# Performance work log

Hardware: AMD Instinct MI355X
Metric: run time of the kernel (lower is better)

## Reference

```python
import jax, jax.numpy as jnp
import numpy as np

N_NODES = 100000
N_EDGES = 1600000
IN_CH = 128
HID_CH = 128
OUT_CH = 128
EDGE_DIM = 16
EPS = 1e-12


def _xavier(key, shape):
    fan_in, fan_out = shape[1], shape[0]
    a = jnp.sqrt(6.0 / (fan_in + fan_out))
    # torch Linear weight is [out, in]; we store transposed [in, out] for x @ W
    return jax.random.uniform(key, (shape[1], shape[0]), minval=-a, maxval=a, dtype=jnp.float32)


def setup_inputs() -> dict:
    key = jax.random.key(0)
    ks = jax.random.split(key, 8)
    x = jax.random.normal(ks[0], (N_NODES, IN_CH), dtype=jnp.float32)
    edge_index = jax.random.randint(ks[1], (2, N_EDGES), 0, N_NODES, dtype=jnp.int64)
    edge_attr = jax.random.normal(ks[2], (N_EDGES, EDGE_DIM), dtype=jnp.float32)
    # layer 1: message Linear(in+edge_dim -> hid), update Linear(in+hid -> hid)
    w_msg1 = _xavier(ks[3], (HID_CH, IN_CH + EDGE_DIM))
    b_msg1 = jnp.zeros((HID_CH,), jnp.float32)
    w_upd1 = _xavier(ks[4], (HID_CH, IN_CH + HID_CH))
    b_upd1 = jnp.zeros((HID_CH,), jnp.float32)
    bias1 = jnp.zeros((HID_CH,), jnp.float32)
    # layer 2: message Linear(hid+edge_dim -> out), update Linear(hid+out -> out)
    w_msg2 = _xavier(ks[5], (OUT_CH, HID_CH + EDGE_DIM))
    b_msg2 = jnp.zeros((OUT_CH,), jnp.float32)
    w_upd2 = _xavier(ks[6], (OUT_CH, HID_CH + OUT_CH))
    b_upd2 = jnp.zeros((OUT_CH,), jnp.float32)
    bias2 = jnp.zeros((OUT_CH,), jnp.float32)
    return {
        "x": x, "edge_index": edge_index, "edge_attr": edge_attr,
        "w_msg1": w_msg1, "b_msg1": b_msg1, "w_upd1": w_upd1, "b_upd1": b_upd1, "bias1": bias1,
        "w_msg2": w_msg2, "b_msg2": b_msg2, "w_upd2": w_upd2, "b_upd2": b_upd2, "bias2": bias2,
    }


def _layer(x, src, dst, edge_attr, w_msg, b_msg, w_upd, b_upd, bias):
    n = x.shape[0]
    # message: gather source node feats, concat edge feats, Linear + ReLU
    msg_in = jnp.concatenate([x[src], edge_attr], axis=1)        # [E, in+edge_dim]
    msg = jax.nn.relu(msg_in @ w_msg + b_msg)                     # [E, out]
    # scatter-mean aggregate at destination nodes
    summed = jax.ops.segment_sum(msg, dst, num_segments=n)        # [N, out]
    cnt = jax.ops.segment_sum(jnp.ones((msg.shape[0], 1), msg.dtype), dst, num_segments=n)
    agg = summed / jnp.maximum(cnt, 1.0)
    # update: concat self feats + aggregated, Linear
    out = jnp.concatenate([x, agg], axis=1) @ w_upd + b_upd       # [N, out]
    # F.normalize(p=2, dim=-1)
    norm = jnp.linalg.norm(out, axis=-1, keepdims=True)
    out = out / jnp.maximum(norm, EPS)
    return out + bias


def reference(x, edge_index, edge_attr,
              w_msg1, b_msg1, w_upd1, b_upd1, bias1,
              w_msg2, b_msg2, w_upd2, b_upd2, bias2):
    src, dst = edge_index[0], edge_index[1]
    h = _layer(x, src, dst, edge_attr, w_msg1, b_msg1, w_upd1, b_upd1, bias1)
    h = jax.nn.relu(h)  # inter-layer ReLU (dropout p=0.0 is identity)
    h = _layer(h, src, dst, edge_attr, w_msg2, b_msg2, w_upd2, b_upd2, bias2)
    return h
```

## Files before the change

kernel.cpp:

```cpp
#include <hip/hip_runtime.h>
#include <stdint.h>

#define N_NODES 100000
#define N_EDGES 1600000
#define CH 128
#define EDGE_DIM 16
#define KUPD 256
#define NPW 8

typedef __attribute__((ext_vector_type(8))) short short8v;
typedef __attribute__((ext_vector_type(4))) float f32x4;

__device__ __forceinline__ float bf2f(ushort u) {
  union { uint i; float f; } c; c.i = ((uint)u) << 16; return c.f;
}
__device__ __forceinline__ ushort f2bf(float f) {
  union { float f; uint i; } c; c.f = f;
  return (ushort)((c.i + 0x7FFFu + ((c.i >> 16) & 1u)) >> 16);
}
__device__ __forceinline__ float ldf(const void* p, int f32, size_t i) {
  return f32 ? ((const float*)p)[i] : bf2f(((const ushort*)p)[i]);
}
__device__ __forceinline__ float2 ld2(const void* p, int f32, size_t pi) {
  if (f32) return ((const float2*)p)[pi];
  uint u = ((const uint*)p)[pi];
  return make_float2(bf2f((ushort)(u & 0xFFFF)), bf2f((ushort)(u >> 16)));
}
__device__ __forceinline__ float4 ld4(const void* p, int f32, size_t qi) {
  if (f32) return ((const float4*)p)[qi];
  uint2 u = ((const uint2*)p)[qi];
  float4 r;
  r.x = bf2f((ushort)(u.x & 0xFFFF)); r.y = bf2f((ushort)(u.x >> 16));
  r.z = bf2f((ushort)(u.y & 0xFFFF)); r.w = bf2f((ushort)(u.y >> 16));
  return r;
}
__device__ __forceinline__ int resolve_f32(int x_sel, const int* flags) {
  return (x_sel == 2) ? 1 : (x_sel == 1 ? flags[1] : 0);
}
__device__ __forceinline__ int kmap(int MAP, int g, int j, int step) {
  return MAP ? (step * 32 + 8 * g + j)
             : (step * 32 + 16 * (j >> 2) + 4 * g + (j & 3));
}

__global__ __launch_bounds__(256) void detect_kernel(const int* __restrict__ ei,
                                                     const ushort* __restrict__ xu,
                                                     const ushort* __restrict__ eau,
                                                     const ushort* __restrict__ wu,
                                                     int* __restrict__ flags) {
  int any = 0, fx = 0, fe = 0, fw = 0;
  for (int i = threadIdx.x; i < 4096; i += 256) any |= ei[2 * i + 1];
  for (int i = threadIdx.x; i < 16384; i += 256) {
    fx |= (((xu[2 * i] >> 7) & 0xFF) == 0xFF);
    fe |= (((eau[2 * i] >> 7) & 0xFF) == 0xFF);
  }
  for (int i = threadIdx.x; i < 8192; i += 256) {
    fw |= (((wu[2 * i] >> 7) & 0xFF) == 0xFF);
  }
  if (any) atomicOr(flags + 0, 1);
  if (fx)  atomicOr(flags + 1, 1);
  if (fe)  atomicOr(flags + 2, 1);
  if (fw)  atomicOr(flags + 3, 1);
}

__global__ __launch_bounds__(64) void mfma_probe(int* __restrict__ flags) {
  __shared__ ushort A[16 * 32];
  __shared__ ushort B[32 * 16];
  const int lane = threadIdx.x;
  for (int idx = lane; idx < 512; idx += 64) {
    int i = idx >> 5, k = idx & 31;
    A[idx] = f2bf((float)((i * 5 + k * 3) % 13 - 6));
    int k2 = idx >> 4, c = idx & 15;
    B[idx] = f2bf((float)((k2 * 7 + c * 11) % 15 - 7));
  }
  __syncthreads();
  const int col = lane & 15, g = lane >> 4;
  float cr[4];
#pragma unroll
  for (int r = 0; r < 4; ++r) {
    int row = g * 4 + r;
    float s = 0.f;
    for (int k = 0; k < 32; ++k) s += bf2f(A[row * 32 + k]) * bf2f(B[k * 16 + col]);
    cr[r] = s;
  }
  int win = 2;
  for (int MAP = 0; MAP < 2; ++MAP) {
    if (win != 2) break;
    short8v a, b;
#pragma unroll
    for (int j = 0; j < 8; ++j) {
      int k = kmap(MAP, g, j, 0);
      a[j] = (short)A[(lane & 15) * 32 + k];
      b[j] = (short)B[k * 16 + col];
    }
    f32x4 z = {0.f, 0.f, 0.f, 0.f};
    f32x4 d = __builtin_amdgcn_mfma_f32_16x16x32_bf16(a, b, z, 0, 0, 0);
    int good = 1;
#pragma unroll
    for (int r = 0; r < 4; ++r) good &= (d[r] == cr[r]);
    if (__all(good)) win = MAP;
  }
  if (lane == 0) flags[4] = win;
}

__device__ __forceinline__ void load_edge(const int* __restrict__ ei, int i32, int e,
                                          int& s, int& d) {
  if (i32) { s = ei[e]; d = ei[N_EDGES + e]; }
  else     { s = ei[2 * e]; d = ei[2 * N_EDGES + 2 * e]; }
  s = min(max(s, 0), N_NODES - 1);
  d = min(max(d, 0), N_NODES - 1);
}

__global__ __launch_bounds__(256) void count_kernel(const int* __restrict__ ei,
                                                    const int* __restrict__ flags,
                                                    int* __restrict__ cnt) {
  int e = blockIdx.x * 256 + threadIdx.x;
  if (e >= N_EDGES) return;
  int d = flags[0] ? ei[N_EDGES + e] : ei[2 * N_EDGES + 2 * e];
  d = min(max(d, 0), N_NODES - 1);
  atomicAdd(&cnt[d], 1);
}

__global__ __launch_bounds__(1024) void scan_kernel(const int* __restrict__ cnt,
                                                    int* __restrict__ rowptr) {
  __shared__ int part[1024];
  const int t = threadIdx.x;
  const int CHUNK = (N_NODES + 1023) / 1024;
  int base = t * CHUNK;
  int lim = min(base + CHUNK, N_NODES);
  int s = 0;
  for (int i = base; i < lim; ++i) s += cnt[i];
  part[t] = s;
  __syncthreads();
  for (int off = 1; off < 1024; off <<= 1) {
    int v = (t >= off) ? part[t - off] : 0;
    __syncthreads();
    part[t] += v;
    __syncthreads();
  }
  int excl = (t == 0) ? 0 : part[t - 1];
  for (int i = base; i < lim; ++i) { rowptr[i] = excl; excl += cnt[i]; }
  if (t == 1023) rowptr[N_NODES] = part[1023];
}

__global__ __launch_bounds__(256) void scatter_kernel(const int* __restrict__ ei,
                                                      const int* __restrict__ flags,
                                                      const int* __restrict__ rowptr,
                                                      int* __restrict__ fill,
                                                      int2* __restrict__ sev) {
  int e = blockIdx.x * 256 + threadIdx.x;
  if (e >= N_EDGES) return;
  int s, d;
  load_edge(ei, flags[0], e, s, d);
  int pos = atomicAdd(&fill[d], 1);
  sev[rowptr[d] + pos] = make_int2(s, e);
}

__global__ __launch_bounds__(256) void wshuf_all(const void* __restrict__ wu1,
                                                 const void* __restrict__ wu2,
                                                 const void* __restrict__ wm1,
                                                 const void* __restrict__ wm2,
                                                 const int* __restrict__ flags,
                                                 ushort* __restrict__ ou1,
                                                 ushort* __restrict__ ou2,
                                                 ushort* __restrict__ om1,
                                                 ushort* __restrict__ om2,
                                                 ushort* __restrict__ oz1,
                                                 ushort* __restrict__ oz2) {
  const int MAP = flags[4], wf = flags[3];
  if (MAP == 2) return;
  int tid = blockIdx.x * 256 + threadIdx.x;
  if (tid >= 13312) return;
  int gg = tid >> 6, lane = tid & 63;
  int col16 = lane & 15, g = lane >> 4;
  if (gg >= 192) {
    int l = gg - 192;
    const void* W = (l < 8) ? wm1 : wm2;
    ushort* dst = (l < 8) ? oz1 : oz2;
    int t = l & 7;
#pragma unroll
    for (int j = 0; j < 8; ++j) {
      int k = kmap(MAP, g, j, 0);
      ushort v = (k < 16) ? f2bf(ldf(W, wf, (size_t)(CH + k) * CH + t * 16 + col16)) : (ushort)0;
      dst[(size_t)t * 512 + lane * 8 + j] = v;
    }
    return;
  }
  const void* W; ushort* dst; int t, step, ts;
  if (gg < 64)       { W = wu1; dst = ou1; int l = gg;       t = l >> 3; step = l & 7; ts = t * 8 + step; }
  else if (gg < 128) { W = wu2; dst = ou2; int l = gg - 64;  t = l >> 3; step = l & 7; ts = t * 8 + step; }
  else if (gg < 160) { W = wm1; dst = om1; int l = gg - 128; t = l >> 2; step = l & 3; ts = t * 4 + step; }
  else               { W = wm2; dst = om2; int l = gg - 160; t = l >> 2; step = l & 3; ts = t * 4 + step; }
  int col = t * 16 + col16;
#pragma unroll
  for (int j = 0; j < 8; ++j) {
    int k = kmap(MAP, g, j, step);
    dst[(size_t)ts * 512 + lane * 8 + j] = f2bf(ldf(W, wf, (size_t)k * CH + col));
  }
}

template <int MAP>
__device__ __forceinline__ void gemm_mfma_body(const void* __restrict__ x, int xf,
                                               const ushort* __restrict__ wshm,
                                               const void* __restrict__ bmsg, int wf,
                                               uint* __restrict__ ybf,
                                               int n0, int lane, char* lds) {
  const int srow = lane >> 2;
  const int q = lane & 3;
  {
    uint sw = (uint)((srow & 7) << 4);
#pragma unroll
    for (int i = 0; i < 8; ++i) {
      int qi = q + 4 * i;
      float4 v = ld4(x, xf, (size_t)(n0 + srow) * 32 + qi);
      uint2 pk;
      pk.x = (uint)f2bf(v.x) | ((uint)f2bf(v.y) << 16);
      pk.y = (uint)f2bf(v.z) | ((uint)f2bf(v.w) << 16);
      *(uint2*)(lds + (((uint)srow * 256u + (uint)qi * 8u) ^ sw)) = pk;
    }
  }
  asm volatile("s_waitcnt lgkmcnt(0)" ::: "memory");
  __builtin_amdgcn_sched_barrier(0);

  const int col = lane & 15, g = lane >> 4;
  const int ra = lane & 15;
  const uint asw = (uint)((ra & 7) << 4);
  f32x4 acc[8];
#pragma unroll
  for (int t = 0; t < 8; ++t) acc[t] = (f32x4){0.f, 0.f, 0.f, 0.f};

#pragma unroll
  for (int step = 0; step < 4; ++step) {
    short8v a;
    if (MAP) {
      uint byte = (uint)ra * 256u + (uint)(step * 32 + 8 * g) * 2u;
      *(uint4*)&a = *(const uint4*)(lds + (byte ^ asw));
    } else {
      uint b0 = (uint)ra * 256u + (uint)(step * 32 + 4 * g) * 2u;
      uint b1 = b0 + 32u;
      uint2 lo = *(const uint2*)(lds + (b0 ^ asw));
      uint2 hi = *(const uint2*)(lds + (b1 ^ asw));
      uint4 pk = make_uint4(lo.x, lo.y, hi.x, hi.y);
      *(uint4*)&a = pk;
    }
#pragma unroll
    for (int t = 0; t < 8; ++t) {
      short8v b = *(const short8v*)(wshm + ((size_t)(t * 4 + step) * 512 + lane * 8));
      acc[t] = __builtin_amdgcn_mfma_f32_16x16x32_bf16(a, b, acc[t], 0, 0, 0);
    }
  }

#pragma unroll
  for (int u = 0; u < 4; ++u) {
    float b0v = ldf(bmsg, wf, u * 32 + col);
    float b1v = ldf(bmsg, wf, u * 32 + 16 + col);
#pragma unroll
    for (int r = 0; r < 4; ++r) {
      uint pk = (uint)f2bf(acc[2 * u][r] + b0v) | ((uint)f2bf(acc[2 * u + 1][r] + b1v) << 16);
      ybf[(uint)(n0 + g * 4 + r) * 64u + (uint)(u * 16 + col)] = pk;
    }
  }
}

__device__ __forceinline__ void gemm_f32_body(const void* __restrict__ x, int xf,
                                              const void* __restrict__ W, int wf,
                                              const void* __restrict__ b,
                                              uint* __restrict__ ybf,
                                              int wave_n0, int lane, char* ldsc) {
  float* xs = (float*)ldsc;
  for (int c = 0; c < 2; ++c) {
    int n0 = wave_n0 + c * 8;
#pragma unroll
    for (int r = 0; r < NPW; ++r) {
      float2 a = ld2(x, xf, (size_t)(n0 + r) * 64 + lane);
      xs[r * 128 + 2 * lane]     = a.x;
      xs[r * 128 + 2 * lane + 1] = a.y;
    }
    asm volatile("s_waitcnt lgkmcnt(0)" ::: "memory");
    __builtin_amdgcn_sched_barrier(0);
    float acc0[NPW], acc1[NPW];
#pragma unroll
    for (int r = 0; r < NPW; ++r) { acc0[r] = 0.f; acc1[r] = 0.f; }
#pragma unroll 4
    for (int k = 0; k < CH; k += 2) {
      float2 w0 = ld2(W, wf, (size_t)k * 64 + lane);
      float2 w1 = ld2(W, wf, (size_t)(k + 1) * 64 + lane);
#pragma unroll
      for (int r = 0; r < NPW; ++r) {
        float2 a = *(const float2*)&xs[r * 128 + k];
        acc0[r] += a.x * w0.x;
        acc1[r] += a.x * w0.y;
        acc0[r] += a.y * w1.x;
        acc1[r] += a.y * w1.y;
      }
    }
    float2 bb = ld2(b, wf, lane);
#pragma unroll
    for (int r = 0; r < NPW; ++r) {
      uint pk = (uint)f2bf(acc0[r] + bb.x) | ((uint)f2bf(acc1[r] + bb.y) << 16);
      ybf[(uint)(n0 + r) * 64u + (uint)lane] = pk;
    }
  }
}

__global__ __launch_bounds__(256) void gemm_node(const void* __restrict__ x, int x_sel,
                                                 const ushort* __restrict__ wshm,
                                                 const void* __restrict__ W,
                                                 const void* __restrict__ b,
                                                 const int* __restrict__ flags,
                                                 uint* __restrict__ ybf) {
  __shared__ char lds[16384];
  const int wave = threadIdx.x >> 6;
  const int lane = threadIdx.x & 63;
  const int wid = blockIdx.x * 4 + wave;
  if (wid >= N_NODES / 16) return;
  const int n0 = wid * 16;
  const int xf = resolve_f32(x_sel, flags), wf = flags[3];
  const int MAP = flags[4];
  char* myl = lds + wave * 4096;
  if (MAP == 0)      gemm_mfma_body<0>(x, xf, wshm, b, wf, ybf, n0, lane, myl);
  else if (MAP == 1) gemm_mfma_body<1>(x, xf, wshm, b, wf, ybf, n0, lane, myl);
  else               gemm_f32_body(x, xf, W, wf, b, ybf, n0, lane, myl);
}

template <int MAP>
__device__ __forceinline__ void agg_mfma_body(const uint* __restrict__ ybf,
                                              const void* __restrict__ ea, int ef,
                                              const ushort* __restrict__ wze,
                                              const int* __restrict__ rowptr,
                                              const int2* __restrict__ sev,
                                              float* __restrict__ agg,
                                              int n, int lane) {
  const int col = lane & 15, g = lane >> 4;
  const int beg = rowptr[n], end = rowptr[n + 1];
  if (beg == end) {
    agg[(size_t)n * CH + (size_t)(2 * g) * 16 + col]     = 0.f;
    agg[(size_t)n * CH + (size_t)(2 * g + 1) * 16 + col] = 0.f;
    return;
  }
  short8v bfr[8];
#pragma unroll
  for (int t = 0; t < 8; ++t)
    bfr[t] = *(const short8v*)(wze + ((size_t)t * 512 + lane * 8));

  f32x4 acc[8];
#pragma unroll
  for (int t = 0; t < 8; ++t) acc[t] = (f32x4){0.f, 0.f, 0.f, 0.f};

  for (int j0 = beg; j0 < end; j0 += 16) {
    int jr = j0 + col;
    if (jr > end - 1) jr = end - 1;
    int2 p = sev[jr];
    int e = p.y;
    short8v a;
    if (MAP == 1) {
      if (g < 2) {
        float4 qa = ld4(ea, ef, (size_t)e * 4 + 2 * g);
        float4 qb = ld4(ea, ef, (size_t)e * 4 + 2 * g + 1);
        uint4 pk;
        pk.x = (uint)f2bf(qa.x) | ((uint)f2bf(qa.y) << 16);
        pk.y = (uint)f2bf(qa.z) | ((uint)f2bf(qa.w) << 16);
        pk.z = (uint)f2bf(qb.x) | ((uint)f2bf(qb.y) << 16);
        pk.w = (uint)f2bf(qb.z) | ((uint)f2bf(qb.w) << 16);
        *(uint4*)&a = pk;
      } else {
        *(uint4*)&a = make_uint4(0, 0, 0, 0);
      }
    } else {
      float4 q = ld4(ea, ef, (size_t)e * 4 + g);
      uint4 pk;
      pk.x = (uint)f2bf(q.x) | ((uint)f2bf(q.y) << 16);
      pk.y = (uint)f2bf(q.z) | ((uint)f2bf(q.w) << 16);
      pk.z = 0; pk.w = 0;
      *(uint4*)&a = pk;
    }
    f32x4 zz = {0.f, 0.f, 0.f, 0.f};
    f32x4 zf[8];
#pragma unroll
    for (int t = 0; t < 8; ++t)
      zf[t] = __builtin_amdgcn_mfma_f32_16x16x32_bf16(a, bfr[t], zz, 0, 0, 0);

    int myS = p.x;
#pragma unroll
    for (int r = 0; r < 4; ++r) {
      int slot = g * 4 + r;
      int s = __shfl(myS, slot);
      float valid = (j0 + slot < end) ? 1.f : 0.f;
#pragma unroll
      for (int u = 0; u < 4; ++u) {
        uint yu = ybf[(size_t)s * 64 + (size_t)u * 16 + col];
        float lo = bf2f((ushort)(yu & 0xFFFF));
        float hi = bf2f((ushort)(yu >> 16));
        acc[2 * u][r]     += valid * fmaxf(lo + zf[2 * u][r], 0.f);
        acc[2 * u + 1][r] += valid * fmaxf(hi + zf[2 * u + 1][r], 0.f);
      }
    }
  }
  float part[8];
#pragma unroll
  for (int t = 0; t < 8; ++t) {
    part[t] = (acc[t][0] + acc[t][1]) + (acc[t][2] + acc[t][3]);
    part[t] += __shfl_xor(part[t], 16);
    part[t] += __shfl_xor(part[t], 32);
  }
  agg[(size_t)n * CH + (size_t)(2 * g) * 16 + col]     = part[2 * g];
  agg[(size_t)n * CH + (size_t)(2 * g + 1) * 16 + col] = part[2 * g + 1];
}

__device__ __forceinline__ void agg_f32_body(const uint* __restrict__ ybf,
                                             const void* __restrict__ ea, int ef,
                                             const void* __restrict__ W, int wf,
                                             const int* __restrict__ rowptr,
                                             const int2* __restrict__ sev,
                                             float* __restrict__ agg,
                                             int n, int lane) {
  const int c0 = 2 * lane, c1 = c0 + 1;
  float wex[EDGE_DIM], wey[EDGE_DIM];
#pragma unroll
  for (int k = 0; k < EDGE_DIM; ++k) {
    wex[k] = ldf(W, wf, (size_t)(CH + k) * CH + c0);
    wey[k] = ldf(W, wf, (size_t)(CH + k) * CH + c1);
  }
  const int beg = rowptr[n], end = rowptr[n + 1];
  float acc0 = 0.f, acc1 = 0.f;
  for (int j = beg; j < end; ++j) {
    int2 p = sev[j];
    int s = __builtin_amdgcn_readfirstlane(p.x), e = __builtin_amdgcn_readfirstlane(p.y);
    uint yu = ybf[(size_t)s * 64 + lane];
    float4 q0 = ld4(ea, ef, (size_t)e * 4 + 0);
    float4 q1 = ld4(ea, ef, (size_t)e * 4 + 1);
    float4 q2 = ld4(ea, ef, (size_t)e * 4 + 2);
    float4 q3 = ld4(ea, ef, (size_t)e * 4 + 3);
    float av[16] = {q0.x, q0.y, q0.z, q0.w, q1.x, q1.y, q1.z, q1.w,
                    q2.x, q2.y, q2.z, q2.w, q3.x, q3.y, q3.z, q3.w};
    float z0 = 0.f, z1 = 0.f;
#pragma unroll
    for (int k = 0; k < EDGE_DIM; ++k) {
      z0 += av[k] * wex[k];
      z1 += av[k] * wey[k];
    }
    acc0 += fmaxf(bf2f((ushort)(yu & 0xFFFF)) + z0, 0.f);
    acc1 += fmaxf(bf2f((ushort)(yu >> 16)) + z1, 0.f);
  }
  agg[(size_t)n * CH + c0] = acc0;
  agg[(size_t)n * CH + c1] = acc1;
}

__global__ __launch_bounds__(256) void agg_csr(const uint* __restrict__ ybf,
                                               const void* __restrict__ ea,
                                               const ushort* __restrict__ wze,
                                               const void* __restrict__ W,
                                               const int* __restrict__ rowptr,
                                               const int2* __restrict__ sev,
                                               const int* __restrict__ flags,
                                               float* __restrict__ agg) {
  const int wave = threadIdx.x >> 6;
  const int lane = threadIdx.x & 63;
  const int n = blockIdx.x * 4 + wave;
  const int ef = flags[2], wf = flags[3], MAP = flags[4];
  if (MAP == 0)      agg_mfma_body<0>(ybf, ea, ef, wze, rowptr, sev, agg, n, lane);
  else if (MAP == 1) agg_mfma_body<1>(ybf, ea, ef, wze, rowptr, sev, agg, n, lane);
  else               agg_f32_body(ybf, ea, ef, W, wf, rowptr, sev, agg, n, lane);
}

template <int MAP>
__device__ __forceinline__ void upd_mfma_body(const void* __restrict__ x, int xf,
                                              const float* __restrict__ agg,
                                              const int* __restrict__ rowptr,
                                              const ushort* __restrict__ wsh,
                                              const void* __restrict__ bupd, int wf,
                                              const void* __restrict__ bias,
                                              float* __restrict__ out, int relu,
                                              int n0, int lane, char* lds) {
  const int srow = lane >> 2;
  const int q = lane & 3;
  {
    int c = rowptr[n0 + srow + 1] - rowptr[n0 + srow];
    float inv = 1.f / (float)(c > 1 ? c : 1);
    uint sw = (uint)((srow & 7) << 4);
#pragma unroll
    for (int i = 0; i < 8; ++i) {
      int qi = q + 4 * i;
      float4 v = ld4(x, xf, (size_t)(n0 + srow) * 32 + qi);
      uint2 pk;
      pk.x = (uint)f2bf(v.x) | ((uint)f2bf(v.y) << 16);
      pk.y = (uint)f2bf(v.z) | ((uint)f2bf(v.w) << 16);
      *(uint2*)(lds + (((uint)srow * 512u + (uint)qi * 8u) ^ sw)) = pk;
      float4 w = ((const float4*)agg)[(size_t)(n0 + srow) * 32 + qi];
      uint2 pk2;
      pk2.x = (uint)f2bf(w.x * inv) | ((uint)f2bf(w.y * inv) << 16);
      pk2.y = (uint)f2bf(w.z * inv) | ((uint)f2bf(w.w * inv) << 16);
      *(uint2*)(lds + (((uint)srow * 512u + 256u + (uint)qi * 8u) ^ sw)) = pk2;
    }
  }
  asm volatile("s_waitcnt lgkmcnt(0)" ::: "memory");
  __builtin_amdgcn_sched_barrier(0);

  const int col = lane & 15, g = lane >> 4;
  const int ra = lane & 15;
  const uint asw = (uint)((ra & 7) << 4);
  f32x4 acc[8];
#pragma unroll
  for (int t = 0; t < 8; ++t) acc[t] = (f32x4){0.f, 0.f, 0.f, 0.f};

#pragma unroll
  for (int step = 0; step < 8; ++step) {
    short8v a;
    if (MAP) {
      uint byte = (uint)ra * 512u + (uint)(step * 32 + 8 * g) * 2u;
      *(uint4*)&a = *(const uint4*)(lds + (byte ^ asw));
    } else {
      uint b0 = (uint)ra * 512u + (uint)(step * 32 + 4 * g) * 2u;
      uint b1 = b0 + 32u;
      uint2 lo = *(const uint2*)(lds + (b0 ^ asw));
      uint2 hi = *(const uint2*)(lds + (b1 ^ asw));
      uint4 pk = make_uint4(lo.x, lo.y, hi.x, hi.y);
      *(uint4*)&a = pk;
    }
#pragma unroll
    for (int t = 0; t < 8; ++t) {
      short8v b = *(const short8v*)(wsh + ((size_t)(t * 8 + step) * 512 + lane * 8));
      acc[t] = __builtin_amdgcn_mfma_f32_16x16x32_bf16(a, b, acc[t], 0, 0, 0);
    }
  }

  float bu[8], bi[8];
#pragma unroll
  for (int t = 0; t < 8; ++t) {
    bu[t] = ldf(bupd, wf, t * 16 + col);
    bi[t] = ldf(bias, wf, t * 16 + col);
  }
  float raw[8][4];
  float ss[4] = {0.f, 0.f, 0.f, 0.f};
#pragma unroll
  for (int t = 0; t < 8; ++t)
#pragma unroll
    for (int r = 0; r < 4; ++r) {
      float v = acc[t][r] + bu[t];
      raw[t][r] = v;
      ss[r] += v * v;
    }
#pragma unroll
  for (int r = 0; r < 4; ++r)
#pragma unroll
    for (int o = 1; o < 16; o <<= 1) ss[r] += __shfl_xor(ss[r], o);
#pragma unroll
  for (int r = 0; r < 4; ++r) {
    float inv = 1.0f / fmaxf(sqrtf(ss[r]), 1e-12f);
    int row = g * 4 + r;
#pragma unroll
    for (int t = 0; t < 8; ++t) {
      float o = raw[t][r] * inv + bi[t];
      if (relu) o = fmaxf(o, 0.f);
      out[(size_t)(n0 + row) * CH + t * 16 + col] = o;
    }
  }
}

__device__ __forceinline__ void upd_f32_body(const void* __restrict__ x, int xf,
                                             const float* __restrict__ agg,
                                             const int* __restrict__ rowptr,
                                             const void* __restrict__ W, int wf,
                                             const void* __restrict__ bupd,
                                             const void* __restrict__ bias,
                                             float* __restrict__ out, int relu,
                                             int wave_n0, int lane, char* ldsc) {
  float* xs = (float*)ldsc;
  for (int c = 0; c < 2; ++c) {
    int n0 = wave_n0 + c * 8;
#pragma unroll
    for (int r = 0; r < NPW; ++r) {
      int n = n0 + r;
      float2 a = ld2(x, xf, (size_t)n * 64 + lane);
      xs[r * 256 + 2 * lane]     = a.x;
      xs[r * 256 + 2 * lane + 1] = a.y;
      int cd = rowptr[n + 1] - rowptr[n];
      float inv = 1.f / (float)(cd > 1 ? cd : 1);
      xs[r * 256 + CH + 2 * lane]     = agg[(size_t)n * CH + 2 * lane] * inv;
      xs[r * 256 + CH + 2 * lane + 1] = agg[(size_t)n * CH + 2 * lane + 1] * inv;
    }
    asm volatile("s_waitcnt lgkmcnt(0)" ::: "memory");
    __builtin_amdgcn_sched_barrier(0);

    float acc0[NPW], acc1[NPW];
#pragma unroll
    for (int r = 0; r < NPW; ++r) { acc0[r] = 0.f; acc1[r] = 0.f; }
#pragma unroll 4
    for (int k = 0; k < KUPD; k += 2) {
      float2 w0 = ld2(W, wf, (size_t)k * 64 + lane);
      float2 w1 = ld2(W, wf, (size_t)(k + 1) * 64 + lane);
#pragma unroll
      for (int r = 0; r < NPW; ++r) {
        float2 a = *(const float2*)&xs[r * 256 + k];
        acc0[r] += a.x * w0.x;
        acc1[r] += a.x * w0.y;
        acc0[r] += a.y * w1.x;
        acc1[r] += a.y * w1.y;
      }
    }
    float2 b  = ld2(bupd, wf, lane);
    float2 bi = ld2(bias, wf, lane);
#pragma unroll
    for (int r = 0; r < NPW; ++r) {
      float r0 = acc0[r] + b.x;
      float r1 = acc1[r] + b.y;
      float sq = r0 * r0 + r1 * r1;
#pragma unroll
      for (int o = 32; o; o >>= 1) sq += __shfl_xor(sq, o);
      float innv = 1.0f / fmaxf(sqrtf(sq), 1e-12f);
      float o0 = r0 * innv + bi.x;
      float o1 = r1 * innv + bi.y;
      if (relu) { o0 = fmaxf(o0, 0.f); o1 = fmaxf(o1, 0.f); }
      size_t n = (size_t)(n0 + r);
      out[n * CH + 2 * lane]     = o0;
      out[n * CH + 2 * lane + 1] = o1;
    }
  }
}

__global__ __launch_bounds__(256) void upd_fused(const void* __restrict__ x, int x_sel,
                                                 const float* __restrict__ agg,
                                                 const int* __restrict__ rowptr,
                                                 const ushort* __restrict__ wsh,
                                                 const void* __restrict__ W,
                                                 const void* __restrict__ bupd,
                                                 const void* __restrict__ bias,
                                                 const int* __restrict__ flags,
                                                 float* __restrict__ out,
                                                 int relu) {
  __shared__ char lds[32768];
  const int wave = threadIdx.x >> 6;
  const int lane = threadIdx.x & 63;
  const int wid = blockIdx.x * 4 + wave;
  if (wid >= N_NODES / 16) return;
  const int n0 = wid * 16;
  const int xf = resolve_f32(x_sel, flags), wf = flags[3];
  const int MAP = flags[4];
  char* myl = lds + wave * 8192;
  if (MAP == 0)
    upd_mfma_body<0>(x, xf, agg, rowptr, wsh, bupd, wf, bias, out, relu, n0, lane, myl);
  else if (MAP == 1)
    upd_mfma_body<1>(x, xf, agg, rowptr, wsh, bupd, wf, bias, out, relu, n0, lane, myl);
  else
    upd_f32_body(x, xf, agg, rowptr, W, wf, bupd, bias, out, relu, n0, lane, myl);
}

extern "C" void kernel_launch(void* const* d_in, const int* in_sizes, int n_in,
                              void* d_out, int out_size, void* d_ws, size_t ws_size,
                              hipStream_t stream) {
  const void* x   = d_in[0];
  const int*  ei  = (const int*)d_in[1];
  const void* ea  = d_in[2];
  const void* wm1 = d_in[3];
  const void* bm1 = d_in[4];
  const void* wu1 = d_in[5];
  const void* bu1 = d_in[6];
  const void* bi1 = d_in[7];
  const void* wm2 = d_in[8];
  const void* bm2 = d_in[9];
  const void* wu2 = d_in[10];
  const void* bu2 = d_in[11];
  const void* bi2 = d_in[12];
  float* out = (float*)d_out;

  char* base = (char*)d_ws;
  size_t off = 0;
  auto alloc = [&](size_t b) { size_t o = off; off += (b + 255) & ~(size_t)255; return o; };
  size_t flags_o = alloc(32);
  size_t cnt_o   = alloc((size_t)N_NODES * 4);
  size_t fill_o  = alloc((size_t)N_NODES * 4);
  size_t zero_end = off;
  size_t rowp_o  = alloc((size_t)(N_NODES + 1) * 4);
  size_t sev_o   = alloc((size_t)N_EDGES * 8);
  size_t agg_o   = alloc((size_t)N_NODES * CH * 4);
  size_t y_o     = alloc((size_t)N_NODES * CH * 2);
  size_t wsh1_o  = alloc((size_t)4096 * 8 * 2);
  size_t wsh2_o  = alloc((size_t)4096 * 8 * 2);
  size_t wshm1_o = alloc((size_t)2048 * 8 * 2);
  size_t wshm2_o = alloc((size_t)2048 * 8 * 2);
  size_t wze1_o  = alloc((size_t)512 * 8 * 2);
  size_t wze2_o  = alloc((size_t)512 * 8 * 2);
  (void)ws_size; (void)n_in; (void)in_sizes; (void)out_size;

  int*    flags = (int*)(base + flags_o);
  int*    cntp  = (int*)(base + cnt_o);
  int*    fillp = (int*)(base + fill_o);
  int*    rowp  = (int*)(base + rowp_o);
  int2*   sevp  = (int2*)(base + sev_o);
  float*  aggp  = (float*)(base + agg_o);
  uint*   ybfp  = (uint*)(base + y_o);
  ushort* wsh1  = (ushort*)(base + wsh1_o);
  ushort* wsh2  = (ushort*)(base + wsh2_o);
  ushort* wshm1 = (ushort*)(base + wshm1_o);
  ushort* wshm2 = (ushort*)(base + wshm2_o);
  ushort* wze1  = (ushort*)(base + wze1_o);
  ushort* wze2  = (ushort*)(base + wze2_o);
  float*  hp    = out;

  hipMemsetAsync(base, 0, zero_end, stream);
  detect_kernel<<<1, 256, 0, stream>>>(ei, (const ushort*)x, (const ushort*)ea,
                                       (const ushort*)wm1, flags);
  mfma_probe<<<1, 64, 0, stream>>>(flags);
  count_kernel<<<(N_EDGES + 255) / 256, 256, 0, stream>>>(ei, flags, cntp);
  scan_kernel<<<1, 1024, 0, stream>>>(cntp, rowp);
  scatter_kernel<<<(N_EDGES + 255) / 256, 256, 0, stream>>>(ei, flags, rowp, fillp, sevp);
  wshuf_all<<<52, 256, 0, stream>>>(wu1, wu2, wm1, wm2, flags,
                                    wsh1, wsh2, wshm1, wshm2, wze1, wze2);

  const int agrid = N_NODES / 4;
  const int wgrid = (N_NODES / 16 + 3) / 4;

  gemm_node<<<wgrid, 256, 0, stream>>>(x, 1, wshm1, wm1, bm1, flags, ybfp);
  agg_csr<<<agrid, 256, 0, stream>>>(ybfp, ea, wze1, wm1, rowp, sevp, flags, aggp);
  upd_fused<<<wgrid, 256, 0, stream>>>(x, 1, aggp, rowp, wsh1, wu1, bu1, bi1, flags, hp, 1);

  gemm_node<<<wgrid, 256, 0, stream>>>(hp, 2, wshm2, wm2, bm2, flags, ybfp);
  agg_csr<<<agrid, 256, 0, stream>>>(ybfp, ea, wze2, wm2, rowp, sevp, flags, aggp);
  upd_fused<<<wgrid, 256, 0, stream>>>(hp, 2, aggp, rowp, wsh2, wu2, bu2, bi2, flags, out, 0);
}
```

Baseline: 1.007 ms.

## Process eight nodes per wave in aggregation and merge probe kernels

The CSR aggregation kernel now has each wave loop over eight consecutive destination nodes instead of one. The per-wave edge-weight fragments are loaded once and reused across those nodes, and the grid shrinks accordingly. Invalid padded edge slots are redirected to an extra zeroed sentinel row of the message buffer, and their edge-attribute operands are masked, so the per-element validity multiply goes away. The detect and MFMA-probe kernels are fused into one launch to save a kernel launch. The trade-off is fewer waves in flight, with per-wave load imbalance across nodes of different degree and serialised node latency.

```diff
diff --git a/kernel.cpp b/kernel.cpp
--- a/kernel.cpp
+++ b/kernel.cpp
@@ -42,11 +42,13 @@
              : (step * 32 + 16 * (j >> 2) + 4 * g + (j & 3));
 }
 
-__global__ __launch_bounds__(256) void detect_kernel(const int* __restrict__ ei,
-                                                     const ushort* __restrict__ xu,
-                                                     const ushort* __restrict__ eau,
-                                                     const ushort* __restrict__ wu,
-                                                     int* __restrict__ flags) {
+__global__ __launch_bounds__(256) void detect_probe(const int* __restrict__ ei,
+                                                    const ushort* __restrict__ xu,
+                                                    const ushort* __restrict__ eau,
+                                                    const ushort* __restrict__ wu,
+                                                    int* __restrict__ flags) {
+  __shared__ ushort A[16 * 32];
+  __shared__ ushort B[32 * 16];
   int any = 0, fx = 0, fe = 0, fw = 0;
   for (int i = threadIdx.x; i < 4096; i += 256) any |= ei[2 * i + 1];
   for (int i = threadIdx.x; i < 16384; i += 256) {
@@ -60,46 +62,43 @@
   if (fx)  atomicOr(flags + 1, 1);
   if (fe)  atomicOr(flags + 2, 1);
   if (fw)  atomicOr(flags + 3, 1);
-}
-
-__global__ __launch_bounds__(64) void mfma_probe(int* __restrict__ flags) {
-  __shared__ ushort A[16 * 32];
-  __shared__ ushort B[32 * 16];
-  const int lane = threadIdx.x;
-  for (int idx = lane; idx < 512; idx += 64) {
+  for (int idx = threadIdx.x; idx < 512; idx += 256) {
     int i = idx >> 5, k = idx & 31;
     A[idx] = f2bf((float)((i * 5 + k * 3) % 13 - 6));
     int k2 = idx >> 4, c = idx & 15;
     B[idx] = f2bf((float)((k2 * 7 + c * 11) % 15 - 7));
   }
   __syncthreads();
-  const int col = lane & 15, g = lane >> 4;
-  float cr[4];
-#pragma unroll
-  for (int r = 0; r < 4; ++r) {
-    int row = g * 4 + r;
-    float s = 0.f;
-    for (int k = 0; k < 32; ++k) s += bf2f(A[row * 32 + k]) * bf2f(B[k * 16 + col]);
-    cr[r] = s;
-  }
-  int win = 2;
-  for (int MAP = 0; MAP < 2; ++MAP) {
-    if (win != 2) break;
-    short8v a, b;
-#pragma unroll
-    for (int j = 0; j < 8; ++j) {
-      int k = kmap(MAP, g, j, 0);
-      a[j] = (short)A[(lane & 15) * 32 + k];
-      b[j] = (short)B[k * 16 + col];
-    }
-    f32x4 z = {0.f, 0.f, 0.f, 0.f};
-    f32x4 d = __builtin_amdgcn_mfma_f32_16x16x32_bf16(a, b, z, 0, 0, 0);
-    int good = 1;
-#pragma unroll
-    for (int r = 0; r < 4; ++r) good &= (d[r] == cr[r]);
-    if (__all(good)) win = MAP;
-  }
-  if (lane == 0) flags[4] = win;
+  if (threadIdx.x < 64) {
+    const int lane = threadIdx.x;
+    const int col = lane & 15, g = lane >> 4;
+    float cr[4];
+#pragma unroll
+    for (int r = 0; r < 4; ++r) {
+      int row = g * 4 + r;
+      float s = 0.f;
+      for (int k = 0; k < 32; ++k) s += bf2f(A[row * 32 + k]) * bf2f(B[k * 16 + col]);
+      cr[r] = s;
+    }
+    int win = 2;
+    for (int MAP = 0; MAP < 2; ++MAP) {
+      if (win != 2) break;
+      short8v a, b;
+#pragma unroll
+      for (int j = 0; j < 8; ++j) {
+        int k = kmap(MAP, g, j, 0);
+        a[j] = (short)A[(lane & 15) * 32 + k];
+        b[j] = (short)B[k * 16 + col];
+      }
+      f32x4 z = {0.f, 0.f, 0.f, 0.f};
+      f32x4 d = __builtin_amdgcn_mfma_f32_16x16x32_bf16(a, b, z, 0, 0, 0);
+      int good = 1;
+#pragma unroll
+      for (int r = 0; r < 4; ++r) good &= (d[r] == cr[r]);
+      if (__all(good)) win = MAP;
+    }
+    if (lane == 0) flags[4] = win;
+  }
 }
 
 __device__ __forceinline__ void load_edge(const int* __restrict__ ei, int i32, int e,
@@ -165,13 +164,18 @@
                                                  ushort* __restrict__ om1,
                                                  ushort* __restrict__ om2,
                                                  ushort* __restrict__ oz1,
-                                                 ushort* __restrict__ oz2) {
+                                                 ushort* __restrict__ oz2,
+                                                 uint* __restrict__ ybf) {
   const int MAP = flags[4], wf = flags[3];
   if (MAP == 2) return;
   int tid = blockIdx.x * 256 + threadIdx.x;
-  if (tid >= 13312) return;
+  if (tid >= 13376) return;
   int gg = tid >> 6, lane = tid & 63;
   int col16 = lane & 15, g = lane >> 4;
+  if (gg == 208) {
+    ybf[(size_t)N_NODES * 64 + lane] = 0u;
+    return;
+  }
   if (gg >= 192) {
     int l = gg - 192;
     const void* W = (l < 8) ? wm1 : wm2;
@@ -329,81 +333,81 @@
                                               const int* __restrict__ rowptr,
                                               const int2* __restrict__ sev,
                                               float* __restrict__ agg,
-                                              int n, int lane) {
+                                              int n0, int lane) {
   const int col = lane & 15, g = lane >> 4;
-  const int beg = rowptr[n], end = rowptr[n + 1];
-  if (beg == end) {
-    agg[(size_t)n * CH + (size_t)(2 * g) * 16 + col]     = 0.f;
-    agg[(size_t)n * CH + (size_t)(2 * g + 1) * 16 + col] = 0.f;
-    return;
-  }
   short8v bfr[8];
 #pragma unroll
   for (int t = 0; t < 8; ++t)
     bfr[t] = *(const short8v*)(wze + ((size_t)t * 512 + lane * 8));
 
-  f32x4 acc[8];
-#pragma unroll
-  for (int t = 0; t < 8; ++t) acc[t] = (f32x4){0.f, 0.f, 0.f, 0.f};
-
-  for (int j0 = beg; j0 < end; j0 += 16) {
-    int jr = j0 + col;
-    if (jr > end - 1) jr = end - 1;
-    int2 p = sev[jr];
-    int e = p.y;
-    short8v a;
-    if (MAP == 1) {
-      if (g < 2) {
-        float4 qa = ld4(ea, ef, (size_t)e * 4 + 2 * g);
-        float4 qb = ld4(ea, ef, (size_t)e * 4 + 2 * g + 1);
+  for (int ni = 0; ni < 8; ++ni) {
+    const int n = n0 + ni;
+    const int beg = rowptr[n], end = rowptr[n + 1];
+    f32x4 acc[8];
+#pragma unroll
+    for (int t = 0; t < 8; ++t) acc[t] = (f32x4){0.f, 0.f, 0.f, 0.f};
+
+    for (int j0 = beg; j0 < end; j0 += 16) {
+      int jr = j0 + col;
+      uint amask = (jr < end) ? 0xFFFFFFFFu : 0u;
+      if (jr > end - 1) jr = end - 1;
+      int2 p = sev[jr];
+      int e = p.y;
+      short8v a;
+      if (MAP == 1) {
+        if (g < 2) {
+          float4 qa = ld4(ea, ef, (size_t)e * 4 + 2 * g);
+          float4 qb = ld4(ea, ef, (size_t)e * 4 + 2 * g + 1);
+          uint4 pk;
+          pk.x = ((uint)f2bf(qa.x) | ((uint)f2bf(qa.y) << 16)) & amask;
+          pk.y = ((uint)f2bf(qa.z) | ((uint)f2bf(qa.w) << 16)) & amask;
+          pk.z = ((uint)f2bf(qb.x) | ((uint)f2bf(qb.y) << 16)) & amask;
+          pk.w = ((uint)f2bf(qb.z) | ((uint)f2bf(qb.w) << 16)) & amask;
+          *(uint4*)&a = pk;
+        } else {
+          *(uint4*)&a = make_uint4(0, 0, 0, 0);
+        }
+      } else {
+        float4 q = ld4(ea, ef, (size_t)e * 4 + g);
         uint4 pk;
-        pk.x = (uint)f2bf(qa.x) | ((uint)f2bf(qa.y) << 16);
-        pk.y = (uint)f2bf(qa.z) | ((uint)f2bf(qa.w) << 16);
-        pk.z = (uint)f2bf(qb.x) | ((uint)f2bf(qb.y) << 16);
-        pk.w = (uint)f2bf(qb.z) | ((uint)f2bf(qb.w) << 16);
+        pk.x = ((uint)f2bf(q.x) | ((uint)f2bf(q.y) << 16)) & amask;
+        pk.y = ((uint)f2bf(q.z) | ((uint)f2bf(q.w) << 16)) & amask;
+        pk.z = 0; pk.w = 0;
         *(uint4*)&a = pk;
-      } else {
-        *(uint4*)&a = make_uint4(0, 0, 0, 0);
       }
-    } else {
-      float4 q = ld4(ea, ef, (size_t)e * 4 + g);
-      uint4 pk;
-      pk.x = (uint)f2bf(q.x) | ((uint)f2bf(q.y) << 16);
-      pk.y = (uint)f2bf(q.z) | ((uint)f2bf(q.w) << 16);
-      pk.z = 0; pk.w = 0;
-      *(uint4*)&a = pk;
-    }
-    f32x4 zz = {0.f, 0.f, 0.f, 0.f};
-    f32x4 zf[8];
-#pragma unroll
-    for (int t = 0; t < 8; ++t)
-      zf[t] = __builtin_amdgcn_mfma_f32_16x16x32_bf16(a, bfr[t], zz, 0, 0, 0);
-
-    int myS = p.x;
-#pragma unroll
-    for (int r = 0; r < 4; ++r) {
-      int slot = g * 4 + r;
-      int s = __shfl(myS, slot);
-      float valid = (j0 + slot < end) ? 1.f : 0.f;
-#pragma unroll
-      for (int u = 0; u < 4; ++u) {
-        uint yu = ybf[(size_t)s * 64 + (size_t)u * 16 + col];
-        float lo = bf2f((ushort)(yu & 0xFFFF));
-        float hi = bf2f((ushort)(yu >> 16));
-        acc[2 * u][r]     += valid * fmaxf(lo + zf[2 * u][r], 0.f);
-        acc[2 * u + 1][r] += valid * fmaxf(hi + zf[2 * u + 1][r], 0.f);
+      f32x4 zz = {0.f, 0.f, 0.f, 0.f};
+      f32x4 zf[8];
+#pragma unroll
+      for (int t = 0; t < 8; ++t)
+        zf[t] = __builtin_amdgcn_mfma_f32_16x16x32_bf16(a, bfr[t], zz, 0, 0, 0);
+
+      int myS = p.x;
+#pragma unroll
+      for (int r = 0; r < 4; ++r) {
+        int slot = g * 4 + r;
+        int s = __shfl(myS, slot);
+        if (j0 + slot >= end) s = N_NODES;
+        uint yb = (uint)s * 64u + (uint)col;
+#pragma unroll
+        for (int u = 0; u < 4; ++u) {
+          uint yu = ybf[yb + (uint)u * 16u];
+          float lo = bf2f((ushort)(yu & 0xFFFF));
+          float hi = bf2f((ushort)(yu >> 16));
+          acc[2 * u][r]     += fmaxf(lo + zf[2 * u][r], 0.f);
+          acc[2 * u + 1][r] += fmaxf(hi + zf[2 * u + 1][r], 0.f);
+        }
       }
     }
-  }
-  float part[8];
-#pragma unroll
-  for (int t = 0; t < 8; ++t) {
-    part[t] = (acc[t][0] + acc[t][1]) + (acc[t][2] + acc[t][3]);
-    part[t] += __shfl_xor(part[t], 16);
-    part[t] += __shfl_xor(part[t], 32);
-  }
-  agg[(size_t)n * CH + (size_t)(2 * g) * 16 + col]     = part[2 * g];
-  agg[(size_t)n * CH + (size_t)(2 * g + 1) * 16 + col] = part[2 * g + 1];
+    float part[8];
+#pragma unroll
+    for (int t = 0; t < 8; ++t) {
+      part[t] = (acc[t][0] + acc[t][1]) + (acc[t][2] + acc[t][3]);
+      part[t] += __shfl_xor(part[t], 16);
+      part[t] += __shfl_xor(part[t], 32);
+    }
+    agg[(size_t)n * CH + (size_t)(2 * g) * 16 + col]     = part[2 * g];
+    agg[(size_t)n * CH + (size_t)(2 * g + 1) * 16 + col] = part[2 * g + 1];
+  }
 }
 
 __device__ __forceinline__ void agg_f32_body(const uint* __restrict__ ybf,
@@ -412,7 +416,7 @@
                                              const int* __restrict__ rowptr,
                                              const int2* __restrict__ sev,
                                              float* __restrict__ agg,
-                                             int n, int lane) {
+                                             int n0, int lane) {
   const int c0 = 2 * lane, c1 = c0 + 1;
   float wex[EDGE_DIM], wey[EDGE_DIM];
 #pragma unroll
@@ -420,29 +424,32 @@
     wex[k] = ldf(W, wf, (size_t)(CH + k) * CH + c0);
     wey[k] = ldf(W, wf, (size_t)(CH + k) * CH + c1);
   }
-  const int beg = rowptr[n], end = rowptr[n + 1];
-  float acc0 = 0.f, acc1 = 0.f;
-  for (int j = beg; j < end; ++j) {
-    int2 p = sev[j];
-    int s = __builtin_amdgcn_readfirstlane(p.x), e = __builtin_amdgcn_readfirstlane(p.y);
-    uint yu = ybf[(size_t)s * 64 + lane];
-    float4 q0 = ld4(ea, ef, (size_t)e * 4 + 0);
-    float4 q1 = ld4(ea, ef, (size_t)e * 4 + 1);
-    float4 q2 = ld4(ea, ef, (size_t)e * 4 + 2);
-    float4 q3 = ld4(ea, ef, (size_t)e * 4 + 3);
-    float av[16] = {q0.x, q0.y, q0.z, q0.w, q1.x, q1.y, q1.z, q1.w,
-                    q2.x, q2.y, q2.z, q2.w, q3.x, q3.y, q3.z, q3.w};
-    float z0 = 0.f, z1 = 0.f;
-#pragma unroll
-    for (int k = 0; k < EDGE_DIM; ++k) {
-      z0 += av[k] * wex[k];
-      z1 += av[k] * wey[k];
-    }
-    acc0 += fmaxf(bf2f((ushort)(yu & 0xFFFF)) + z0, 0.f);
-    acc1 += fmaxf(bf2f((ushort)(yu >> 16)) + z1, 0.f);
-  }
-  agg[(size_t)n * CH + c0] = acc0;
-  agg[(size_t)n * CH + c1] = acc1;
+  for (int ni = 0; ni < 8; ++ni) {
+    const int n = n0 + ni;
+    const int beg = rowptr[n], end = rowptr[n + 1];
+    float acc0 = 0.f, acc1 = 0.f;
+    for (int j = beg; j < end; ++j) {
+      int2 p = sev[j];
+      int s = __builtin_amdgcn_readfirstlane(p.x), e = __builtin_amdgcn_readfirstlane(p.y);
+      uint yu = ybf[(size_t)s * 64 + lane];
+      float4 q0 = ld4(ea, ef, (size_t)e * 4 + 0);
+      float4 q1 = ld4(ea, ef, (size_t)e * 4 + 1);
+      float4 q2 = ld4(ea, ef, (size_t)e * 4 + 2);
+      float4 q3 = ld4(ea, ef, (size_t)e * 4 + 3);
+      float av[16] = {q0.x, q0.y, q0.z, q0.w, q1.x, q1.y, q1.z, q1.w,
+                      q2.x, q2.y, q2.z, q2.w, q3.x, q3.y, q3.z, q3.w};
+      float z0 = 0.f, z1 = 0.f;
+#pragma unroll
+      for (int k = 0; k < EDGE_DIM; ++k) {
+        z0 += av[k] * wex[k];
+        z1 += av[k] * wey[k];
+      }
+      acc0 += fmaxf(bf2f((ushort)(yu & 0xFFFF)) + z0, 0.f);
+      acc1 += fmaxf(bf2f((ushort)(yu >> 16)) + z1, 0.f);
+    }
+    agg[(size_t)n * CH + c0] = acc0;
+    agg[(size_t)n * CH + c1] = acc1;
+  }
 }
 
 __global__ __launch_bounds__(256) void agg_csr(const uint* __restrict__ ybf,
@@ -455,11 +462,11 @@
                                                float* __restrict__ agg) {
   const int wave = threadIdx.x >> 6;
   const int lane = threadIdx.x & 63;
-  const int n = blockIdx.x * 4 + wave;
+  const int n0 = (blockIdx.x * 4 + wave) * 8;
   const int ef = flags[2], wf = flags[3], MAP = flags[4];
-  if (MAP == 0)      agg_mfma_body<0>(ybf, ea, ef, wze, rowptr, sev, agg, n, lane);
-  else if (MAP == 1) agg_mfma_body<1>(ybf, ea, ef, wze, rowptr, sev, agg, n, lane);
-  else               agg_f32_body(ybf, ea, ef, W, wf, rowptr, sev, agg, n, lane);
+  if (MAP == 0)      agg_mfma_body<0>(ybf, ea, ef, wze, rowptr, sev, agg, n0, lane);
+  else if (MAP == 1) agg_mfma_body<1>(ybf, ea, ef, wze, rowptr, sev, agg, n0, lane);
+  else               agg_f32_body(ybf, ea, ef, W, wf, rowptr, sev, agg, n0, lane);
 }
 
 template <int MAP>
@@ -672,7 +679,7 @@
   size_t rowp_o  = alloc((size_t)(N_NODES + 1) * 4);
   size_t sev_o   = alloc((size_t)N_EDGES * 8);
   size_t agg_o   = alloc((size_t)N_NODES * CH * 4);
-  size_t y_o     = alloc((size_t)N_NODES * CH * 2);
+  size_t y_o     = alloc((size_t)(N_NODES + 1) * CH * 2);
   size_t wsh1_o  = alloc((size_t)4096 * 8 * 2);
   size_t wsh2_o  = alloc((size_t)4096 * 8 * 2);
   size_t wshm1_o = alloc((size_t)2048 * 8 * 2);
@@ -697,16 +704,15 @@
   float*  hp    = out;
 
   hipMemsetAsync(base, 0, zero_end, stream);
-  detect_kernel<<<1, 256, 0, stream>>>(ei, (const ushort*)x, (const ushort*)ea,
-                                       (const ushort*)wm1, flags);
-  mfma_probe<<<1, 64, 0, stream>>>(flags);
+  detect_probe<<<1, 256, 0, stream>>>(ei, (const ushort*)x, (const ushort*)ea,
+                                      (const ushort*)wm1, flags);
   count_kernel<<<(N_EDGES + 255) / 256, 256, 0, stream>>>(ei, flags, cntp);
   scan_kernel<<<1, 1024, 0, stream>>>(cntp, rowp);
   scatter_kernel<<<(N_EDGES + 255) / 256, 256, 0, stream>>>(ei, flags, rowp, fillp, sevp);
-  wshuf_all<<<52, 256, 0, stream>>>(wu1, wu2, wm1, wm2, flags,
-                                    wsh1, wsh2, wshm1, wshm2, wze1, wze2);
-
-  const int agrid = N_NODES / 4;
+  wshuf_all<<<53, 256, 0, stream>>>(wu1, wu2, wm1, wm2, flags,
+                                    wsh1, wsh2, wshm1, wshm2, wze1, wze2, ybfp);
+
+  const int agrid = N_NODES / 32;
   const int wgrid = (N_NODES / 16 + 3) / 4;
 
   gemm_node<<<wgrid, 256, 0, stream>>>(x, 1, wshm1, wm1, bm1, flags, ybfp);
```

New measurement: 968.5 us. -3.8%, faster.
